# Kernel tuning notes

Hardware: AMD Instinct MI355X
Metric: run time of the kernel (lower is better)

## Reference

```python
import jax, jax.numpy as jnp
import numpy as np

D = 1024
K_LOW1 = D // 4  # first low-precision segment of the contraction dim
K_LOW2 = D // 4  # last low-precision segment


def mix_precision_matmul(x, w):
    """x: [B,N,d], w: [d,3d]. Contraction dim d is split into
    low1 | high | low2 column bands; low bands run in fp16, high in fp32.
    Partial products are summed to give the full matmul result."""
    d = x.shape[-1]
    w1 = w[:K_LOW1]
    wh = w[K_LOW1:d - K_LOW2]
    w2 = w[d - K_LOW2:]
    y1 = jnp.matmul(x[..., :K_LOW1].astype(jnp.float16), w1.astype(jnp.float16)).astype(jnp.float32)
    yh = jnp.matmul(x[..., K_LOW1:d - K_LOW2], wh)
    y2 = jnp.matmul(x[..., d - K_LOW2:].astype(jnp.float16), w2.astype(jnp.float16)).astype(jnp.float32)
    return y1 + yh + y2


def setup_inputs() -> dict:
    key = jax.random.key(0)
    k1, k2, k3, k4 = jax.random.split(key, 4)
    B, N, d = 8, 2048, D
    x = jax.random.normal(k1, (B, N, d), dtype=jnp.float32)
    weight_qkv = jax.random.normal(k2, (d, 3 * d), dtype=jnp.float32) * (d ** -0.5)
    out_w = jax.random.normal(k3, (d, d), dtype=jnp.float32) * (d ** -0.5)
    out_b = jax.random.normal(k4, (d,), dtype=jnp.float32) * 0.01
    return {"x": x, "weight_qkv": weight_qkv, "out_w": out_w, "out_b": out_b}


def reference(x, weight_qkv, out_w, out_b):
    d = x.shape[-1]
    qkv = mix_precision_matmul(x, weight_qkv)  # [B, N, 3d]
    q, k, v = jnp.split(qkv, 3, axis=-1)
    q = q / jnp.sqrt(jnp.asarray(d, dtype=q.dtype))
    qk = jnp.einsum('bqd,bkd->bqk', q, k)      # [B, N, N]
    s = jax.nn.softmax(qk, axis=-1)
    y = jnp.einsum('bqk,bkd->bqd', s, v)       # [B, N, d]
    return jnp.matmul(y, out_w.T) + out_b
```

## Files before the change

kernel.cpp:

```cpp
#include <hip/hip_runtime.h>

typedef __attribute__((ext_vector_type(8))) _Float16 half8;
typedef __attribute__((ext_vector_type(4))) _Float16 half4;
typedef __attribute__((ext_vector_type(4))) float floatx4;

#define DEVI __device__ __forceinline__

DEVI void gload_lds16(const _Float16* g, _Float16* l) {
    __builtin_amdgcn_global_load_lds(
        (const __attribute__((address_space(1))) void*)g,
        (__attribute__((address_space(3))) void*)l, 16, 0, 0);
}

#define WAITV(N) asm volatile("s_waitcnt vmcnt(" #N ")" ::: "memory")
#define BAR() __builtin_amdgcn_s_barrier()


template <int K>
DEVI void stage_unit(const _Float16* __restrict__ src, _Float16* dst, int tid) {
    const int s0 = tid, s1 = tid + 512;
    const int r0 = s0 >> 3, c0 = (s0 & 7) ^ (r0 & 7);
    const int r1 = s1 >> 3, c1 = (s1 & 7) ^ (r1 & 7);
    gload_lds16(src + (size_t)r0 * K + c0 * 8, dst + s0 * 8);
    gload_lds16(src + (size_t)r1 * K + c1 * 8, dst + s1 * 8);
}

template <int K>
DEVI void stage_u(const _Float16* __restrict__ A, const _Float16* __restrict__ B,
                  _Float16* lds, int t, int u, int tid) {
    constexpr int NT = K >> 6;
    const int tt = t < NT ? t : NT - 1;
    const _Float16* sp = ((u < 2) ? A : B) + (size_t)((u & 1) * 128) * K + (size_t)tt * 64;
    stage_unit<K>(sp, lds + ((t & 1) * 4 + u) * 8192, tid);
}

template <int K>
DEVI void gemm8p(const _Float16* __restrict__ A, const _Float16* __restrict__ B,
                 _Float16* lds, floatx4 acc[8][4], int tid)
{
    const int lane = tid & 63, w = tid >> 6;
    const int wm = w >> 2, wn = w & 3;
    const int lr = lane & 15, quad = lane >> 4, xr = lr & 7;
    const int co0 = (quad ^ xr) << 3;
    const int co1 = ((4 + quad) ^ xr) << 3;
    const int brow = (wn & 1) * 64;
    const int aU = wm, bU = 2 + (wn >> 1);
    constexpr int NT = K >> 6;

    stage_u<K>(A, B, lds, 0, 0, tid); stage_u<K>(A, B, lds, 0, 1, tid);
    stage_u<K>(A, B, lds, 0, 2, tid); stage_u<K>(A, B, lds, 0, 3, tid);
    stage_u<K>(A, B, lds, 1, 2, tid); stage_u<K>(A, B, lds, 1, 3, tid);
    WAITV(4);
    BAR();

    for (int T = 0; T < NT; ++T) {
        const _Float16* ua = lds + ((T & 1) * 4 + aU) * 8192;
        const _Float16* ub = lds + ((T & 1) * 4 + bU) * 8192;
        half8 bf[4][2];
#pragma unroll
        for (int q = 0; q < 4; ++q) {
            if (q == 0) {
#pragma unroll
                for (int ni = 0; ni < 4; ++ni) {
                    bf[ni][0] = *(const half8*)&ub[(brow + ni * 16 + lr) * 64 + co0];
                    bf[ni][1] = *(const half8*)&ub[(brow + ni * 16 + lr) * 64 + co1];
                }
            }
            half8 af[2][2];
#pragma unroll
            for (int m2 = 0; m2 < 2; ++m2) {
                af[m2][0] = *(const half8*)&ua[(q * 32 + m2 * 16 + lr) * 64 + co0];
                af[m2][1] = *(const half8*)&ua[(q * 32 + m2 * 16 + lr) * 64 + co1];
            }
            if      (q == 0) stage_u<K>(A, B, lds, T + 1, 0, tid);
            else if (q == 1) stage_u<K>(A, B, lds, T + 1, 1, tid);
            else if (q == 2) stage_u<K>(A, B, lds, T + 2, 2, tid);
            else           { stage_u<K>(A, B, lds, T + 2, 3, tid); WAITV(4); }
            BAR();
            __builtin_amdgcn_s_setprio(1);
#pragma unroll
            for (int kk = 0; kk < 2; ++kk)
#pragma unroll
                for (int m2 = 0; m2 < 2; ++m2)
#pragma unroll
                    for (int ni = 0; ni < 4; ++ni)
                        acc[2 * q + m2][ni] = __builtin_amdgcn_mfma_f32_16x16x32_f16(
                            af[m2][kk], bf[ni][kk], acc[2 * q + m2][ni], 0, 0, 0);
            __builtin_amdgcn_s_setprio(0);
            BAR();
        }
    }
    WAITV(0);
}

DEVI void zacc(floatx4 acc[8][4]) {
    const floatx4 zf = {0.f, 0.f, 0.f, 0.f};
#pragma unroll
    for (int mi = 0; mi < 8; ++mi)
#pragma unroll
        for (int ni = 0; ni < 4; ++ni) acc[mi][ni] = zf;
}

__global__ __launch_bounds__(256) void k_cast_x(const float* __restrict__ x, _Float16* __restrict__ xh) {
    size_t i = ((size_t)blockIdx.x * 256 + threadIdx.x) * 8;
    float4 v0 = *(const float4*)(x + i);
    float4 v1 = *(const float4*)(x + i + 4);
    float vv[8] = {v0.x, v0.y, v0.z, v0.w, v1.x, v1.y, v1.z, v1.w};
    half8 h;
#pragma unroll
    for (int j = 0; j < 8; ++j) h[j] = (_Float16)vv[j];
    *(half8*)(xh + i) = h;
}

__global__ __launch_bounds__(256) void k_prep_w(const float* __restrict__ w, _Float16* __restrict__ wh) {
    __shared__ float tile[32][33];
    const int n0 = blockIdx.x * 32, k0 = blockIdx.y * 32;
    const int t = threadIdx.x;
#pragma unroll
    for (int it = 0; it < 4; ++it) {
        int idx = it * 256 + t;
        int kk = idx >> 5, nn = idx & 31;
        tile[kk][nn] = w[(size_t)(k0 + kk) * 3072 + n0 + nn];
    }
    __syncthreads();
#pragma unroll
    for (int it = 0; it < 4; ++it) {
        int idx = it * 256 + t;
        int nn = idx >> 5, kk = idx & 31;
        wh[(size_t)(n0 + nn) * 1024 + k0 + kk] = (_Float16)tile[kk][nn];
    }
}

__global__ __launch_bounds__(256) void k_prep_ow(const float* __restrict__ ow, _Float16* __restrict__ owh) {
    size_t i = ((size_t)blockIdx.x * 256 + threadIdx.x) * 8;
    float4 v0 = *(const float4*)(ow + i);
    float4 v1 = *(const float4*)(ow + i + 4);
    float vv[8] = {v0.x, v0.y, v0.z, v0.w, v1.x, v1.y, v1.z, v1.w};
    half8 h;
#pragma unroll
    for (int j = 0; j < 8; ++j) h[j] = (_Float16)vv[j];
    *(half8*)(owh + i) = h;
}

__global__ __launch_bounds__(512, 2) void k_qkv256(
    const _Float16* __restrict__ xh, const _Float16* __restrict__ wh,
    _Float16* __restrict__ qh, _Float16* __restrict__ kh, _Float16* __restrict__ vT)
{
    __shared__ __align__(16) _Float16 L[65536];
    const int lin = blockIdx.x + 64 * blockIdx.y;
    const int xcd = lin & 7, j = lin >> 3;
    const int m0 = (xcd * 8 + (j & 7)) * 256, n0 = (j >> 3) * 256;
    const int tid = threadIdx.x;
    floatx4 acc[8][4];
    zacc(acc);
    gemm8p<1024>(xh + (size_t)m0 * 1024, wh + (size_t)n0 * 1024, L, acc, tid);

    const int lane = tid & 63, w = tid >> 6;
    const int lr = lane & 15, quad = lane >> 4;
    const int mb0 = m0 + (w >> 2) * 128 + quad * 4;
    const int nb0 = n0 + (w & 3) * 64 + lr;
    if (n0 < 1024) {
#pragma unroll
        for (int mi = 0; mi < 8; ++mi)
#pragma unroll
            for (int ni = 0; ni < 4; ++ni)
#pragma unroll
                for (int r = 0; r < 4; ++r)
                    qh[(size_t)(mb0 + mi * 16 + r) * 1024 + (nb0 + ni * 16)] =
                        (_Float16)(acc[mi][ni][r] * 0.03125f);
    } else if (n0 < 2048) {
#pragma unroll
        for (int mi = 0; mi < 8; ++mi)
#pragma unroll
            for (int ni = 0; ni < 4; ++ni)
#pragma unroll
                for (int r = 0; r < 4; ++r)
                    kh[(size_t)(mb0 + mi * 16 + r) * 1024 + (nb0 - 1024 + ni * 16)] =
                        (_Float16)acc[mi][ni][r];
    } else {
#pragma unroll
        for (int mi = 0; mi < 8; ++mi)
#pragma unroll
            for (int ni = 0; ni < 4; ++ni) {
                int mb = mb0 + mi * 16;
                int b = mb >> 11, ml = mb & 2047;
                int e = nb0 - 2048 + ni * 16;
                half4 pk;
#pragma unroll
                for (int r = 0; r < 4; ++r) pk[r] = (_Float16)acc[mi][ni][r];
                *(half4*)&vT[((size_t)b * 1024 + e) * 2048 + ml] = pk;
            }
    }
}

template <int EPI, int K, int MODE>
__global__ __launch_bounds__(512, 2) void k_g256(
    const _Float16* __restrict__ Ab, const _Float16* __restrict__ Bb,
    _Float16* __restrict__ C16, float* __restrict__ C32, const float* __restrict__ bias,
    unsigned long long sAz, unsigned long long sBz, unsigned long long sCz, int ldc)
{
    __shared__ __align__(16) _Float16 L[65536];
    const int gx = gridDim.x, gy = gridDim.y;
    const int lin = blockIdx.x + gx * (blockIdx.y + gy * blockIdx.z);
    const int xcd = lin & 7, j = lin >> 3;
    int bx, by, bz;
    if (MODE == 0) { bz = xcd; bx = j % gx; by = j / gx; }
    else           { bz = 0;   bx = xcd * (gx >> 3) + j % (gx >> 3); by = j / (gx >> 3); }
    const int m0 = bx * 256, n0 = by * 256;
    const int tid = threadIdx.x;
    floatx4 acc[8][4];
    zacc(acc);
    gemm8p<K>(Ab + (size_t)bz * sAz + (size_t)m0 * K,
              Bb + (size_t)bz * sBz + (size_t)n0 * K, L, acc, tid);

    const int lane = tid & 63, w = tid >> 6;
    const int lr = lane & 15, quad = lane >> 4;
    const int mb0 = m0 + (w >> 2) * 128 + quad * 4;
    const int nb0 = n0 + (w & 3) * 64 + lr;
#pragma unroll
    for (int mi = 0; mi < 8; ++mi)
#pragma unroll
        for (int ni = 0; ni < 4; ++ni)
#pragma unroll
            for (int r = 0; r < 4; ++r) {
                int m = mb0 + mi * 16 + r;
                int n = nb0 + ni * 16;
                if (EPI == 0)
                    C16[(size_t)bz * sCz + (size_t)m * ldc + n] = (_Float16)acc[mi][ni][r];
                else
                    C32[(size_t)m * ldc + n] = acc[mi][ni][r] + bias[n];
            }
}

DEVI float wred_max(float v) {
#pragma unroll
    for (int o = 32; o; o >>= 1) v = fmaxf(v, __shfl_xor(v, o, 64));
    return v;
}
DEVI float wred_sum(float v) {
#pragma unroll
    for (int o = 32; o; o >>= 1) v += __shfl_xor(v, o, 64);
    return v;
}

__global__ __launch_bounds__(256) void k_softmax(_Float16* __restrict__ S) {
    const size_t row = blockIdx.x;
    _Float16* p = S + row * 2048;
    const int t = threadIdx.x;
    __shared__ float redm[4], reds[4];
    float v[8];
    float mx = -3.4e38f;
#pragma unroll
    for (int i = 0; i < 8; ++i) { v[i] = (float)p[t + i * 256]; mx = fmaxf(mx, v[i]); }
    mx = wred_max(mx);
    if ((t & 63) == 0) redm[t >> 6] = mx;
    __syncthreads();
    mx = fmaxf(fmaxf(redm[0], redm[1]), fmaxf(redm[2], redm[3]));
    float s = 0.f;
#pragma unroll
    for (int i = 0; i < 8; ++i) { v[i] = __expf(v[i] - mx); s += v[i]; }
    s = wred_sum(s);
    if ((t & 63) == 0) reds[t >> 6] = s;
    __syncthreads();
    s = reds[0] + reds[1] + reds[2] + reds[3];
    float inv = 1.0f / s;
#pragma unroll
    for (int i = 0; i < 8; ++i) p[t + i * 256] = (_Float16)(v[i] * inv);
}

extern "C" void kernel_launch(void* const* d_in, const int* in_sizes, int n_in,
                              void* d_out, int out_size, void* d_ws, size_t ws_size,
                              hipStream_t stream) {
    const float* x  = (const float*)d_in[0];
    const float* wq = (const float*)d_in[1];
    const float* ow = (const float*)d_in[2];
    const float* ob = (const float*)d_in[3];
    float* out = (float*)d_out;

    char* ws = (char*)d_ws;
    _Float16* xh  = (_Float16*)(ws + 0);
    _Float16* wh  = (_Float16*)(ws + 33554432);
    _Float16* S   = (_Float16*)(ws + 0);
    _Float16* qh  = (_Float16*)(ws + 67108864);
    _Float16* kh  = (_Float16*)(ws + 100663296);
    _Float16* vT  = (_Float16*)(ws + 134217728);
    _Float16* owh = (_Float16*)(ws + 167772160);
    _Float16* y   = qh;

    if (ws_size < 180355072ull) return;

    hipLaunchKernelGGL(k_cast_x, dim3(8192), dim3(256), 0, stream, x, xh);
    hipLaunchKernelGGL(k_prep_w, dim3(96, 32), dim3(256), 0, stream, wq, wh);
    hipLaunchKernelGGL(k_qkv256, dim3(64, 12), dim3(512), 0, stream, xh, wh, qh, kh, vT);
    hipLaunchKernelGGL((k_g256<0, 1024, 0>), dim3(8, 8, 8), dim3(512), 0, stream,
                       qh, kh, S, (float*)nullptr, (const float*)nullptr,
                       2048ull * 1024, 2048ull * 1024, 2048ull * 2048, 2048);
    hipLaunchKernelGGL(k_prep_ow, dim3(512), dim3(256), 0, stream, ow, owh);
    hipLaunchKernelGGL(k_softmax, dim3(16384), dim3(256), 0, stream, S);
    hipLaunchKernelGGL((k_g256<0, 2048, 0>), dim3(8, 4, 8), dim3(512), 0, stream,
                       S, vT, y, (float*)nullptr, (const float*)nullptr,
                       2048ull * 2048, 1024ull * 2048, 2048ull * 1024, 1024);
    hipLaunchKernelGGL((k_g256<1, 1024, 1>), dim3(64, 4, 1), dim3(512), 0, stream,
                       y, owh, (_Float16*)nullptr, out, ob,
                       0ull, 0ull, 0ull, 1024);
}
```

Baseline: 431.7 us.

## Replace eight-phase interleaved GEMM pipeline with simple double-buffered K loop

The GEMM main loop used to split each K tile into four quarter-phases, interleaving global-to-LDS staging with fragment loads and MFMAs, with a barrier per phase. It now issues all staging for tile T+1 at the top of each iteration, waits and syncs once, loads all A and B fragments, and runs all MFMAs. This cuts barriers and simplifies scheduling, but loses the fine-grained overlap of loads and compute. It also holds all eight A fragments in registers at once, which raises register pressure and risks spills or lower occupancy.

```diff
diff --git a/kernel.cpp b/kernel.cpp
--- a/kernel.cpp
+++ b/kernel.cpp
@@ -15,15 +15,6 @@
 #define WAITV(N) asm volatile("s_waitcnt vmcnt(" #N ")" ::: "memory")
 #define BAR() __builtin_amdgcn_s_barrier()
 
-
-template <int K>
-DEVI void stage_unit(const _Float16* __restrict__ src, _Float16* dst, int tid) {
-    const int s0 = tid, s1 = tid + 512;
-    const int r0 = s0 >> 3, c0 = (s0 & 7) ^ (r0 & 7);
-    const int r1 = s1 >> 3, c1 = (s1 & 7) ^ (r1 & 7);
-    gload_lds16(src + (size_t)r0 * K + c0 * 8, dst + s0 * 8);
-    gload_lds16(src + (size_t)r1 * K + c1 * 8, dst + s1 * 8);
-}
 
 template <int K>
 DEVI void stage_u(const _Float16* __restrict__ A, const _Float16* __restrict__ B,
@@ -31,11 +22,16 @@
     constexpr int NT = K >> 6;
     const int tt = t < NT ? t : NT - 1;
     const _Float16* sp = ((u < 2) ? A : B) + (size_t)((u & 1) * 128) * K + (size_t)tt * 64;
-    stage_unit<K>(sp, lds + ((t & 1) * 4 + u) * 8192, tid);
+    _Float16* dst = lds + ((t & 1) * 4 + u) * 8192;
+    const int s0 = tid, s1 = tid + 512;
+    const int r0 = s0 >> 3, c0 = (s0 & 7) ^ (r0 & 7);
+    const int r1 = s1 >> 3, c1 = (s1 & 7) ^ (r1 & 7);
+    gload_lds16(sp + (size_t)r0 * K + c0 * 8, dst + s0 * 8);
+    gload_lds16(sp + (size_t)r1 * K + c1 * 8, dst + s1 * 8);
 }
 
 template <int K>
-DEVI void gemm8p(const _Float16* __restrict__ A, const _Float16* __restrict__ B,
+DEVI void gemmdp(const _Float16* __restrict__ A, const _Float16* __restrict__ B,
                  _Float16* lds, floatx4 acc[8][4], int tid)
 {
     const int lane = tid & 63, w = tid >> 6;
@@ -49,46 +45,38 @@
 
     stage_u<K>(A, B, lds, 0, 0, tid); stage_u<K>(A, B, lds, 0, 1, tid);
     stage_u<K>(A, B, lds, 0, 2, tid); stage_u<K>(A, B, lds, 0, 3, tid);
-    stage_u<K>(A, B, lds, 1, 2, tid); stage_u<K>(A, B, lds, 1, 3, tid);
-    WAITV(4);
-    BAR();
 
     for (int T = 0; T < NT; ++T) {
+        stage_u<K>(A, B, lds, T + 1, 0, tid); stage_u<K>(A, B, lds, T + 1, 1, tid);
+        stage_u<K>(A, B, lds, T + 1, 2, tid); stage_u<K>(A, B, lds, T + 1, 3, tid);
+        WAITV(8);
+        BAR();
+
         const _Float16* ua = lds + ((T & 1) * 4 + aU) * 8192;
         const _Float16* ub = lds + ((T & 1) * 4 + bU) * 8192;
         half8 bf[4][2];
 #pragma unroll
-        for (int q = 0; q < 4; ++q) {
-            if (q == 0) {
-#pragma unroll
-                for (int ni = 0; ni < 4; ++ni) {
-                    bf[ni][0] = *(const half8*)&ub[(brow + ni * 16 + lr) * 64 + co0];
-                    bf[ni][1] = *(const half8*)&ub[(brow + ni * 16 + lr) * 64 + co1];
-                }
-            }
-            half8 af[2][2];
-#pragma unroll
-            for (int m2 = 0; m2 < 2; ++m2) {
-                af[m2][0] = *(const half8*)&ua[(q * 32 + m2 * 16 + lr) * 64 + co0];
-                af[m2][1] = *(const half8*)&ua[(q * 32 + m2 * 16 + lr) * 64 + co1];
-            }
-            if      (q == 0) stage_u<K>(A, B, lds, T + 1, 0, tid);
-            else if (q == 1) stage_u<K>(A, B, lds, T + 1, 1, tid);
-            else if (q == 2) stage_u<K>(A, B, lds, T + 2, 2, tid);
-            else           { stage_u<K>(A, B, lds, T + 2, 3, tid); WAITV(4); }
-            BAR();
-            __builtin_amdgcn_s_setprio(1);
+        for (int ni = 0; ni < 4; ++ni) {
+            bf[ni][0] = *(const half8*)&ub[(brow + ni * 16 + lr) * 64 + co0];
+            bf[ni][1] = *(const half8*)&ub[(brow + ni * 16 + lr) * 64 + co1];
+        }
+        half8 af[8][2];
+#pragma unroll
+        for (int mi = 0; mi < 8; ++mi) {
+            af[mi][0] = *(const half8*)&ua[(mi * 16 + lr) * 64 + co0];
+            af[mi][1] = *(const half8*)&ua[(mi * 16 + lr) * 64 + co1];
+        }
+        __builtin_amdgcn_s_setprio(1);
+#pragma unroll
+        for (int mi = 0; mi < 8; ++mi)
 #pragma unroll
             for (int kk = 0; kk < 2; ++kk)
 #pragma unroll
-                for (int m2 = 0; m2 < 2; ++m2)
-#pragma unroll
-                    for (int ni = 0; ni < 4; ++ni)
-                        acc[2 * q + m2][ni] = __builtin_amdgcn_mfma_f32_16x16x32_f16(
-                            af[m2][kk], bf[ni][kk], acc[2 * q + m2][ni], 0, 0, 0);
-            __builtin_amdgcn_s_setprio(0);
-            BAR();
-        }
+                for (int ni = 0; ni < 4; ++ni)
+                    acc[mi][ni] = __builtin_amdgcn_mfma_f32_16x16x32_f16(
+                        af[mi][kk], bf[ni][kk], acc[mi][ni], 0, 0, 0);
+        __builtin_amdgcn_s_setprio(0);
+        BAR();
     }
     WAITV(0);
 }
@@ -153,7 +141,7 @@
     const int tid = threadIdx.x;
     floatx4 acc[8][4];
     zacc(acc);
-    gemm8p<1024>(xh + (size_t)m0 * 1024, wh + (size_t)n0 * 1024, L, acc, tid);
+    gemmdp<1024>(xh + (size_t)m0 * 1024, wh + (size_t)n0 * 1024, L, acc, tid);
 
     const int lane = tid & 63, w = tid >> 6;
     const int lr = lane & 15, quad = lane >> 4;
@@ -210,7 +198,7 @@
     const int tid = threadIdx.x;
     floatx4 acc[8][4];
     zacc(acc);
-    gemm8p<K>(Ab + (size_t)bz * sAz + (size_t)m0 * K,
+    gemmdp<K>(Ab + (size_t)bz * sAz + (size_t)m0 * K,
               Bb + (size_t)bz * sBz + (size_t)n0 * K, L, acc, tid);
 
     const int lane = tid & 63, w = tid >> 6;
```

Measured after the change: 425.3 us. No clear change (-1.5%).
